# Performance work log

Measured on AMD Instinct MI355X. Metric: run time of the kernel, lower is better.

## Reference

```python
import jax, jax.numpy as jnp
import numpy as np

B, L, D, H, K = 4, 2048, 1024, 16, 3
HEAD_DIM = D // H
LN_EPS = 1e-5


def setup_inputs() -> dict:
    key = jax.random.key(0)
    ks = jax.random.split(key, 12)
    w = lambda k, shp: jax.random.normal(k, shp, jnp.float32) * (shp[-1] ** -0.5)
    return {
        "x": jax.random.normal(ks[0], (B, L, D), jnp.float32),
        "band_importance": jax.random.normal(ks[1], (1, L), jnp.float32) * 0.02,
        "Wq": w(ks[2], (D, D)), "bq": jnp.zeros((D,), jnp.float32),
        "Wk": w(ks[3], (D, D)), "bk": jnp.zeros((D,), jnp.float32),
        "Wv": w(ks[4], (D, D)), "bv": jnp.zeros((D,), jnp.float32),
        "Wo": w(ks[5], (D, D)), "bo": jnp.zeros((D,), jnp.float32),
        "gamma": jnp.ones((D,), jnp.float32),
        "beta": jnp.zeros((D,), jnp.float32),
    }


def reference(x, band_importance, Wq, bq, Wk, bk, Wv, bv, Wo, bo, gamma, beta):
    Bx, Lx, Dx = x.shape
    hd = Dx // H
    # top-k over softmax(band_importance); PyTorch bool attn_mask: True = BLOCKED
    imp = jax.nn.softmax(band_importance, axis=-1)[0]            # (L,)
    _, idx = jax.lax.top_k(imp, K)                               # (K,) int
    col_mask = jnp.zeros((Lx,), bool).at[idx].set(True)          # (L,) True -> masked out
    bias = jnp.where(col_mask, -jnp.inf, 0.0).astype(x.dtype)    # (L,)

    q = (x @ Wq.T + bq).reshape(Bx, Lx, H, hd)
    k_ = (x @ Wk.T + bk).reshape(Bx, Lx, H, hd)
    v = (x @ Wv.T + bv).reshape(Bx, Lx, H, hd)

    scale = 1.0 / np.sqrt(hd)
    scores = jnp.einsum("bqhd,bkhd->bhqk", q, k_) * scale + bias[None, None, None, :]
    attn = jax.nn.softmax(scores, axis=-1)                       # (B,H,L,L)
    ctx = jnp.einsum("bhqk,bkhd->bqhd", attn, v).reshape(Bx, Lx, Dx)
    attn_out = ctx @ Wo.T + bo

    y = x + attn_out                                             # residual
    mu = jnp.mean(y, axis=-1, keepdims=True)
    var = jnp.mean((y - mu) ** 2, axis=-1, keepdims=True)
    return (y - mu) * jax.lax.rsqrt(var + LN_EPS) * gamma + beta
```

## Files before the change

kernel.cpp:

```cpp
#include <hip/hip_runtime.h>

#define GAS __attribute__((address_space(1)))
#define LAS __attribute__((address_space(3)))

typedef __attribute__((ext_vector_type(8))) short short8;
typedef __attribute__((ext_vector_type(4))) float f32x4;
typedef __attribute__((ext_vector_type(16))) float f32x16;
typedef __attribute__((ext_vector_type(4))) unsigned int u32x4;

#define MFMA16(a,b,c) __builtin_amdgcn_mfma_f32_16x16x32_bf16(a,b,c,0,0,0)
#define MFMA32(a,b,c) __builtin_amdgcn_mfma_f32_32x32x16_bf16(a,b,c,0,0,0)

__device__ __forceinline__ unsigned short f2b(float f) {
  unsigned u = __float_as_uint(f);
  u += 0x7fffu + ((u >> 16) & 1u);
  return (unsigned short)(u >> 16);
}
__device__ __forceinline__ float b2f(unsigned short h) {
  return __uint_as_float(((unsigned)h) << 16);
}
__device__ __forceinline__ unsigned cvtpk(float a, float b) {
  unsigned r;
  asm("v_cvt_pk_bf16_f32 %0, %1, %2" : "=v"(r) : "v"(a), "v"(b));
  return r;
}
__device__ __forceinline__ void pl32swap(unsigned &x, unsigned &y) {
  auto r = __builtin_amdgcn_permlane32_swap((int)x, (int)y, false, false);
  x = (unsigned)r[0]; y = (unsigned)r[1];
}
__device__ __forceinline__ float xhalf_sum(float v) {
  auto r = __builtin_amdgcn_permlane32_swap(__float_as_int(v), __float_as_int(v), false, false);
  return __int_as_float(r[0]) + __int_as_float(r[1]);
}
__device__ __forceinline__ float fexp2(float x) {
  float r;
  asm("v_exp_f32 %0, %1" : "=v"(r) : "v"(x));
  return r;
}

union FW { u32x4 u; short8 s; };

__global__ void cvt_all(const float* __restrict__ x,
                        const float* __restrict__ Wq, const float* __restrict__ Wk,
                        const float* __restrict__ Wv, const float* __restrict__ Wo,
                        unsigned short* __restrict__ xb,
                        unsigned short* __restrict__ Wqkvb,
                        unsigned short* __restrict__ Wob) {
  const int bid = blockIdx.x;
  const float* src;
  unsigned short* dst;
  int idx;
  if (bid < 8192) {
    src = x; dst = xb; idx = bid * 256 + threadIdx.x;
  } else {
    int wb = bid - 8192;
    int seg = wb >> 10;
    idx = (wb & 1023) * 256 + threadIdx.x;
    src = (seg == 0) ? Wq : (seg == 1) ? Wk : (seg == 2) ? Wv : Wo;
    dst = (seg == 3) ? Wob : (Wqkvb + (size_t)seg * 1048576);
  }
  float4 v = reinterpret_cast<const float4*>(src)[idx];
  ushort4 o;
  o.x = f2b(v.x); o.y = f2b(v.y); o.z = f2b(v.z); o.w = f2b(v.w);
  reinterpret_cast<ushort4*>(dst)[idx] = o;
}

__global__ void topk_idx(const float* __restrict__ band, int* __restrict__ idxout) {
  __shared__ float svals[256];
  __shared__ int   sidx[256];
  __shared__ int   chosen[3];
  const int t = threadIdx.x;
  for (int pass = 0; pass < 3; ++pass) {
    float best = -INFINITY; int bi = 1 << 30;
    for (int j = t; j < 2048; j += 256) {
      float v = band[j];
      bool skip = false;
      for (int p2 = 0; p2 < pass; ++p2) skip |= (chosen[p2] == j);
      if (!skip && (v > best || (v == best && j < bi))) { best = v; bi = j; }
    }
    svals[t] = best; sidx[t] = bi;
    __syncthreads();
    for (int s = 128; s > 0; s >>= 1) {
      if (t < s) {
        float v2 = svals[t + s]; int i2 = sidx[t + s];
        if (v2 > svals[t] || (v2 == svals[t] && i2 < sidx[t])) { svals[t] = v2; sidx[t] = i2; }
      }
      __syncthreads();
    }
    if (t == 0) chosen[pass] = sidx[0];
    __syncthreads();
  }
  if (t < 3) idxout[t] = chosen[t];
}

__global__ __launch_bounds__(256) void gemm_qkv(
    const unsigned short* __restrict__ A,
    const unsigned short* __restrict__ Wqkv,
    const float* __restrict__ bq, const float* __restrict__ bk,
    const float* __restrict__ bv,
    unsigned short* __restrict__ qout, unsigned short* __restrict__ kout,
    unsigned short* __restrict__ vout, float qscale)
{
  __shared__ short As[128][64];
  __shared__ short Bs[128][64];
  const int tid = threadIdx.x;
  const int w = tid >> 6, lane = tid & 63;
  const int wm = w >> 1, wn = w & 1;
  const int flat = blockIdx.y * 64 + blockIdx.x;
  const int swb = (flat & 7) * 192 + (flat >> 3);
  const int m0 = (swb & 63) * 128, n0 = (swb >> 6) * 128;
  const int rA = lane >> 3, cA = lane & 7;

  const int seg = n0 >> 10;
  const float* biasp = (seg == 0) ? bq : (seg == 1) ? bk : bv;
  unsigned short* outp = (seg == 0) ? qout : (seg == 1) ? kout : vout;
  const float scale = (seg == 0) ? qscale : 1.0f;

  f32x4 acc[4][4];
  #pragma unroll
  for (int mt = 0; mt < 4; ++mt)
    #pragma unroll
    for (int nt = 0; nt < 4; ++nt)
      #pragma unroll
      for (int r = 0; r < 4; ++r) acc[mt][nt][r] = 0.f;

  for (int kt = 0; kt < 16; ++kt) {
    #pragma unroll
    for (int j = 0; j < 4; ++j) {
      int r = w * 32 + j * 8;
      const unsigned short* ga = A + (size_t)(m0 + r + rA) * 1024 + kt * 64 + cA * 8;
      __builtin_amdgcn_global_load_lds((const GAS void*)ga, (LAS void*)&As[r][0], 16, 0, 0);
      const unsigned short* gb = Wqkv + (size_t)(n0 + r + rA) * 1024 + kt * 64 + cA * 8;
      __builtin_amdgcn_global_load_lds((const GAS void*)gb, (LAS void*)&Bs[r][0], 16, 0, 0);
    }
    __syncthreads();
    #pragma unroll
    for (int kc = 0; kc < 2; ++kc) {
      short8 a[4], b[4];
      #pragma unroll
      for (int mt = 0; mt < 4; ++mt)
        a[mt] = *reinterpret_cast<const short8*>(
            &As[wm * 64 + mt * 16 + (lane & 15)][kc * 32 + (lane >> 4) * 8]);
      #pragma unroll
      for (int nt = 0; nt < 4; ++nt)
        b[nt] = *reinterpret_cast<const short8*>(
            &Bs[wn * 64 + nt * 16 + (lane & 15)][kc * 32 + (lane >> 4) * 8]);
      __builtin_amdgcn_s_setprio(1);
      #pragma unroll
      for (int mt = 0; mt < 4; ++mt)
        #pragma unroll
        for (int nt = 0; nt < 4; ++nt)
          acc[mt][nt] = MFMA16(a[mt], b[nt], acc[mt][nt]);
      __builtin_amdgcn_s_setprio(0);
    }
    __syncthreads();
  }
  #pragma unroll
  for (int nt = 0; nt < 4; ++nt) {
    int col = n0 + wn * 64 + nt * 16 + (lane & 15);
    int coll = col & 1023;
    float bval = biasp[coll];
    int h_ = coll >> 6, d_ = coll & 63;
    #pragma unroll
    for (int mt = 0; mt < 4; ++mt) {
      int rbase = m0 + wm * 64 + mt * 16 + ((lane >> 4) << 2);
      #pragma unroll
      for (int r = 0; r < 4; ++r) {
        unsigned short val = f2b((acc[mt][nt][r] + bval) * scale);
        int row = rbase + r;
        int b_ = row >> 11, lt_ = row & 2047;
        outp[(((size_t)(b_ * 16 + h_)) * 2048 + lt_) * 64 + d_] = val;
      }
    }
  }
}

__global__ __launch_bounds__(256) void gemm_wo(
    const unsigned short* __restrict__ A,
    const unsigned short* __restrict__ Bw,
    const float* __restrict__ bias,
    unsigned short* __restrict__ C)
{
  __shared__ short As[128][64];
  __shared__ short Bs[128][64];
  const int tid = threadIdx.x;
  const int w = tid >> 6, lane = tid & 63;
  const int wm = w >> 1, wn = w & 1;
  const int flat = blockIdx.y * 64 + blockIdx.x;
  const int swb = (flat & 7) * 64 + (flat >> 3);
  const int m0 = (swb & 63) * 128, n0 = (swb >> 6) * 128;
  const int rA = lane >> 3, cA = lane & 7;

  f32x4 acc[4][4];
  #pragma unroll
  for (int mt = 0; mt < 4; ++mt)
    #pragma unroll
    for (int nt = 0; nt < 4; ++nt)
      #pragma unroll
      for (int r = 0; r < 4; ++r) acc[mt][nt][r] = 0.f;

  for (int kt = 0; kt < 16; ++kt) {
    #pragma unroll
    for (int j = 0; j < 4; ++j) {
      int r = w * 32 + j * 8;
      const unsigned short* ga = A + (size_t)(m0 + r + rA) * 1024 + kt * 64 + cA * 8;
      __builtin_amdgcn_global_load_lds((const GAS void*)ga, (LAS void*)&As[r][0], 16, 0, 0);
      const unsigned short* gb = Bw + (size_t)(n0 + r + rA) * 1024 + kt * 64 + cA * 8;
      __builtin_amdgcn_global_load_lds((const GAS void*)gb, (LAS void*)&Bs[r][0], 16, 0, 0);
    }
    __syncthreads();
    #pragma unroll
    for (int kc = 0; kc < 2; ++kc) {
      short8 a[4], b[4];
      #pragma unroll
      for (int mt = 0; mt < 4; ++mt)
        a[mt] = *reinterpret_cast<const short8*>(
            &As[wm * 64 + mt * 16 + (lane & 15)][kc * 32 + (lane >> 4) * 8]);
      #pragma unroll
      for (int nt = 0; nt < 4; ++nt)
        b[nt] = *reinterpret_cast<const short8*>(
            &Bs[wn * 64 + nt * 16 + (lane & 15)][kc * 32 + (lane >> 4) * 8]);
      __builtin_amdgcn_s_setprio(1);
      #pragma unroll
      for (int mt = 0; mt < 4; ++mt)
        #pragma unroll
        for (int nt = 0; nt < 4; ++nt)
          acc[mt][nt] = MFMA16(a[mt], b[nt], acc[mt][nt]);
      __builtin_amdgcn_s_setprio(0);
    }
    __syncthreads();
  }
  #pragma unroll
  for (int nt = 0; nt < 4; ++nt) {
    int col = n0 + wn * 64 + nt * 16 + (lane & 15);
    float bval = bias[col];
    #pragma unroll
    for (int mt = 0; mt < 4; ++mt) {
      int rbase = m0 + wm * 64 + mt * 16 + ((lane >> 4) << 2);
      #pragma unroll
      for (int r = 0; r < 4; ++r)
        C[(size_t)(rbase + r) * 1024 + col] = f2b(acc[mt][nt][r] + bval);
    }
  }
}

__global__ __launch_bounds__(256) void transpose_v(
    const unsigned short* __restrict__ vin,
    unsigned short* __restrict__ vout)
{
  __shared__ short T[64 * 64];
  const int lt = blockIdx.x, bh = blockIdx.y;
  const int tid = threadIdx.x;
  #pragma unroll
  for (int p = 0; p < 2; ++p) {
    int id = p * 256 + tid; int l = id >> 3, c = id & 7;
    short8 v = *reinterpret_cast<const short8*>(
        vin + ((size_t)bh * 2048 + lt * 64 + l) * 64 + c * 8);
    *reinterpret_cast<short8*>(&T[l * 64 + ((c ^ (l & 7)) * 8)]) = v;
  }
  __syncthreads();
  #pragma unroll
  for (int p = 0; p < 2; ++p) {
    int id = p * 256 + tid; int d = id >> 3, c2 = id & 7;
    short8 o;
    #pragma unroll
    for (int j = 0; j < 8; ++j) {
      int l = c2 * 8 + j;
      o[j] = T[l * 64 + (((d >> 3) ^ (l & 7)) * 8) + (d & 7)];
    }
    *reinterpret_cast<short8*>(vout + ((size_t)bh * 64 + d) * 2048 + lt * 64 + c2 * 8) = o;
  }
}

#define PACK8(S, j0, OUT) {                                        \
    unsigned A_ = cvtpk(S[(j0)+0], S[(j0)+1]);                     \
    unsigned B_ = cvtpk(S[(j0)+4], S[(j0)+5]);                     \
    unsigned C_ = cvtpk(S[(j0)+2], S[(j0)+3]);                     \
    unsigned D_ = cvtpk(S[(j0)+6], S[(j0)+7]);                     \
    pl32swap(A_, B_); pl32swap(C_, D_);                            \
    FW f_; f_.u[0] = A_; f_.u[1] = C_; f_.u[2] = B_; f_.u[3] = D_; \
    OUT = f_.s; }

__global__ __launch_bounds__(256, 3) void attn4(
    const unsigned short* __restrict__ qg,
    const unsigned short* __restrict__ kg,
    const unsigned short* __restrict__ vtg,
    const int* __restrict__ midx,
    unsigned short* __restrict__ ctx)
{
  __shared__ short Ks[2][64 * 64];
  __shared__ short Vs[2][64 * 64];
  const int tid = threadIdx.x, w = tid >> 6, lane = tid & 63;
  const int flat = blockIdx.y * 16 + blockIdx.x;
  const int swzb = (flat & 7) * 128 + (flat >> 3);
  const int qt = swzb & 15, bh = swzb >> 4;
  const int q0 = qt * 128;
  const int lo5 = lane & 31, hi = lane >> 5;
  const int i0 = midx[0], i1 = midx[1], i2 = midx[2];

  const int qrow = q0 + w * 32 + lo5;
  const unsigned short* qp = qg + ((size_t)bh * 2048 + qrow) * 64 + hi * 8;
  short8 qf[4];
  #pragma unroll
  for (int ds = 0; ds < 4; ++ds) qf[ds] = *reinterpret_cast<const short8*>(qp + ds * 16);

  f32x16 oacc0, oacc1, lacc;
  #pragma unroll
  for (int r = 0; r < 16; ++r) { oacc0[r] = 0.f; oacc1[r] = 0.f; lacc[r] = 0.f; }

  const int swzoff = (((lane & 7) ^ (lane >> 3))) * 8;
  const unsigned short* kp0 =
      kg + ((size_t)bh * 2048 + w * 8 + (lane >> 3)) * 64 + swzoff;
  const unsigned short* kp1 = kp0 + 32 * 64;
  const unsigned short* vp0 =
      vtg + ((size_t)(bh * 64 + w * 8 + (lane >> 3))) * 2048 + swzoff;
  const unsigned short* vp1 = vp0 + 32 * 2048;

#define STAGE_K(bufi, tt) do {                                                 \
    __builtin_amdgcn_global_load_lds((const GAS void*)(kp0 + (tt) * 4096),     \
        (LAS void*)&Ks[bufi][(w * 8) * 64], 16, 0, 0);                         \
    __builtin_amdgcn_global_load_lds((const GAS void*)(kp1 + (tt) * 4096),     \
        (LAS void*)&Ks[bufi][(32 + w * 8) * 64], 16, 0, 0);                    \
  } while (0)
#define STAGE_V(bufi, tt) do {                                                 \
    __builtin_amdgcn_global_load_lds((const GAS void*)(vp0 + (tt) * 64),       \
        (LAS void*)&Vs[bufi][(w * 8) * 64], 16, 0, 0);                         \
    __builtin_amdgcn_global_load_lds((const GAS void*)(vp1 + (tt) * 64),       \
        (LAS void*)&Vs[bufi][(32 + w * 8) * 64], 16, 0, 0);                    \
  } while (0)

  STAGE_K(0, 0); STAGE_V(0, 0);
  STAGE_K(1, 1); STAGE_V(1, 1);

  for (int t = 0; t < 32; ++t) {
    const int buf = t & 1;
    if (t < 31) { asm volatile("s_waitcnt vmcnt(4)" ::: "memory"); }
    else        { asm volatile("s_waitcnt vmcnt(0)" ::: "memory"); }
    __builtin_amdgcn_sched_barrier(0);
    __builtin_amdgcn_s_barrier();
    __builtin_amdgcn_sched_barrier(0);

    short8 kf[8];
    #pragma unroll
    for (int ds = 0; ds < 4; ++ds) {
      int cw = ds * 2 + hi;
      kf[2 * ds] = *reinterpret_cast<const short8*>(
          &Ks[buf][lo5 * 64 + ((cw ^ (lo5 & 7)) * 8)]);
      kf[2 * ds + 1] = *reinterpret_cast<const short8*>(
          &Ks[buf][(32 + lo5) * 64 + ((cw ^ (lo5 & 7)) * 8)]);
    }
    asm volatile("s_waitcnt lgkmcnt(0)" ::: "memory");
    __builtin_amdgcn_sched_barrier(0);
    __builtin_amdgcn_s_barrier();
    __builtin_amdgcn_sched_barrier(0);
    if (t < 30) STAGE_K(buf, t + 2);

    f32x16 s0, s1;
    #pragma unroll
    for (int r = 0; r < 16; ++r) { s0[r] = 0.f; s1[r] = 0.f; }
    __builtin_amdgcn_s_setprio(1);
    #pragma unroll
    for (int ds = 0; ds < 4; ++ds) {
      s0 = MFMA32(kf[2 * ds], qf[ds], s0);
      s1 = MFMA32(kf[2 * ds + 1], qf[ds], s1);
    }
    __builtin_amdgcn_s_setprio(0);

    #pragma unroll
    for (int r = 0; r < 16; ++r) s0[r] = fexp2(s0[r]);
    #pragma unroll
    for (int r = 0; r < 16; ++r) s1[r] = fexp2(s1[r]);

    int t64 = t * 64;
    bool tm = ((unsigned)(i0 - t64) < 64u) | ((unsigned)(i1 - t64) < 64u) |
              ((unsigned)(i2 - t64) < 64u);
    if (tm) {
      #pragma unroll
      for (int r = 0; r < 16; ++r) {
        int kg0 = t64 + (r & 3) + 8 * (r >> 2) + 4 * hi;
        int kg1 = kg0 + 32;
        if (kg0 == i0 || kg0 == i1 || kg0 == i2) s0[r] = 0.f;
        if (kg1 == i0 || kg1 == i1 || kg1 == i2) s1[r] = 0.f;
      }
    }

    #pragma unroll
    for (int r = 0; r < 16; ++r) lacc[r] += s0[r] + s1[r];

    short8 pa[4];
    PACK8(s0, 0, pa[0]); PACK8(s0, 8, pa[1]);
    PACK8(s1, 0, pa[2]); PACK8(s1, 8, pa[3]);

    short8 vf[8];
    #pragma unroll
    for (int ks = 0; ks < 4; ++ks) {
      int cw = ks * 2 + hi;
      vf[2 * ks] = *reinterpret_cast<const short8*>(
          &Vs[buf][lo5 * 64 + ((cw ^ (lo5 & 7)) * 8)]);
      vf[2 * ks + 1] = *reinterpret_cast<const short8*>(
          &Vs[buf][(32 + lo5) * 64 + ((cw ^ (lo5 & 7)) * 8)]);
    }
    asm volatile("s_waitcnt lgkmcnt(0)" ::: "memory");
    __builtin_amdgcn_sched_barrier(0);
    __builtin_amdgcn_s_barrier();
    __builtin_amdgcn_sched_barrier(0);
    if (t < 30) STAGE_V(buf, t + 2);

    __builtin_amdgcn_s_setprio(1);
    #pragma unroll
    for (int ks = 0; ks < 4; ++ks) {
      oacc0 = MFMA32(pa[ks], vf[2 * ks], oacc0);
      oacc1 = MFMA32(pa[ks], vf[2 * ks + 1], oacc1);
    }
    __builtin_amdgcn_s_setprio(0);
  }

  float lsum = 0.f;
  #pragma unroll
  for (int r = 0; r < 16; ++r) lsum += lacc[r];
  lsum = xhalf_sum(lsum);
  const int bb = bh >> 4, hh = bh & 15;
  float rinv = 1.0f / lsum;
  #pragma unroll
  for (int r = 0; r < 16; ++r) {
    int row = (r & 3) + 8 * (r >> 2) + 4 * hi;
    float rv = __int_as_float(__builtin_amdgcn_ds_bpermute(
        (row + (lane & 32)) * 4, __float_as_int(rinv)));
    int qr = q0 + w * 32 + row;
    size_t base = (((size_t)(bb * 2048 + qr)) * 16 + hh) * 64;
    ctx[base + lo5]      = f2b(oacc0[r] * rv);
    ctx[base + 32 + lo5] = f2b(oacc1[r] * rv);
  }
}

__global__ __launch_bounds__(256) void resid_ln(
    const float* __restrict__ x, const unsigned short* __restrict__ ao,
    const float* __restrict__ gamma, const float* __restrict__ beta,
    float* __restrict__ out)
{
  const int row = blockIdx.x, t = threadIdx.x;
  const size_t base = (size_t)row * 1024;
  float4 xv = reinterpret_cast<const float4*>(x + base)[t];
  ushort4 av = reinterpret_cast<const ushort4*>(ao + base)[t];
  float y[4] = {xv.x + b2f(av.x), xv.y + b2f(av.y), xv.z + b2f(av.z), xv.w + b2f(av.w)};
  float sum = y[0] + y[1] + y[2] + y[3];
  float sq = y[0] * y[0] + y[1] * y[1] + y[2] * y[2] + y[3] * y[3];
  #pragma unroll
  for (int off = 1; off < 64; off <<= 1) {
    sum += __shfl_xor(sum, off);
    sq += __shfl_xor(sq, off);
  }
  __shared__ float s1[4], s2[4];
  int w = t >> 6, lane = t & 63;
  if (lane == 0) { s1[w] = sum; s2[w] = sq; }
  __syncthreads();
  sum = s1[0] + s1[1] + s1[2] + s1[3];
  sq = s2[0] + s2[1] + s2[2] + s2[3];
  float mu = sum * (1.f / 1024.f);
  float var = sq * (1.f / 1024.f) - mu * mu;
  float inv = rsqrtf(var + 1e-5f);
  float4 gv = reinterpret_cast<const float4*>(gamma)[t];
  float4 bv = reinterpret_cast<const float4*>(beta)[t];
  float4 o;
  o.x = (y[0] - mu) * inv * gv.x + bv.x;
  o.y = (y[1] - mu) * inv * gv.y + bv.y;
  o.z = (y[2] - mu) * inv * gv.z + bv.z;
  o.w = (y[3] - mu) * inv * gv.w + bv.w;
  reinterpret_cast<float4*>(out + base)[t] = o;
}

extern "C" void kernel_launch(void* const* d_in, const int* in_sizes, int n_in,
                              void* d_out, int out_size, void* d_ws, size_t ws_size,
                              hipStream_t stream)
{
  const float* x     = (const float*)d_in[0];
  const float* band  = (const float*)d_in[1];
  const float* Wq    = (const float*)d_in[2];
  const float* bq    = (const float*)d_in[3];
  const float* Wk    = (const float*)d_in[4];
  const float* bk    = (const float*)d_in[5];
  const float* Wv    = (const float*)d_in[6];
  const float* bv    = (const float*)d_in[7];
  const float* Wo    = (const float*)d_in[8];
  const float* bo    = (const float*)d_in[9];
  const float* gamma = (const float*)d_in[10];
  const float* beta  = (const float*)d_in[11];
  float* out = (float*)d_out;

  char* ws = (char*)d_ws;
  int*            idxw  = (int*)(ws);
  unsigned short* xb    = (unsigned short*)(ws + 4096);
  unsigned short* Wqkvb = (unsigned short*)(ws + 16781312);
  unsigned short* Wob   = (unsigned short*)(ws + 23072768);
  unsigned short* qb    = (unsigned short*)(ws + 25169920);
  unsigned short* kb    = (unsigned short*)(ws + 41947136);
  unsigned short* vhb   = (unsigned short*)(ws + 58724352);
  unsigned short* vtb   = (unsigned short*)(ws + 75501568);
  unsigned short* ctxb  = vhb;
  unsigned short* aob   = qb;

  const float QSCALE = 0.125f * 1.44269504f;

  cvt_all<<<12288, 256, 0, stream>>>(x, Wq, Wk, Wv, Wo, xb, Wqkvb, Wob);
  topk_idx<<<1, 256, 0, stream>>>(band, idxw);

  gemm_qkv<<<dim3(64, 24), 256, 0, stream>>>(xb, Wqkvb, bq, bk, bv,
                                             qb, kb, vhb, QSCALE);

  transpose_v<<<dim3(32, 64), 256, 0, stream>>>(vhb, vtb);

  attn4<<<dim3(16, 64), 256, 0, stream>>>(qb, kb, vtb, idxw, ctxb);

  gemm_wo<<<dim3(64, 8), 256, 0, stream>>>(ctxb, Wob, bo, aob);

  resid_ln<<<8192, 256, 0, stream>>>(x, aob, gamma, beta, out);
}
```

Baseline: 232.4 us.

## Load V fragments directly from global memory and merge top-k into convert kernel

The attention kernel stops staging V tiles through shared memory with async global-to-LDS copies. Each lane now reads its V MFMA fragments straight from global memory, issued before the QK matmul. This drops one barrier per iteration and half the LDS footprint, and the launch bound moves from 3 to 2 blocks per SM. Separately, the top-k index kernel is folded into the bf16 conversion kernel as one extra block, saving a launch. The trade-off is that V loads are no longer double-buffered and their global latency must be hidden by the QK compute, with possibly less coalesced access.

```diff
diff --git a/kernel.cpp b/kernel.cpp
--- a/kernel.cpp
+++ b/kernel.cpp
@@ -37,35 +37,40 @@
   asm("v_exp_f32 %0, %1" : "=v"(r) : "v"(x));
   return r;
 }
+__device__ __forceinline__ short8 ld8(const unsigned short* p) {
+  return *reinterpret_cast<const short8*>(p);
+}
 
 union FW { u32x4 u; short8 s; };
 
-__global__ void cvt_all(const float* __restrict__ x,
-                        const float* __restrict__ Wq, const float* __restrict__ Wk,
-                        const float* __restrict__ Wv, const float* __restrict__ Wo,
-                        unsigned short* __restrict__ xb,
-                        unsigned short* __restrict__ Wqkvb,
-                        unsigned short* __restrict__ Wob) {
+__global__ void cvt_topk(const float* __restrict__ x,
+                         const float* __restrict__ Wq, const float* __restrict__ Wk,
+                         const float* __restrict__ Wv, const float* __restrict__ Wo,
+                         const float* __restrict__ band,
+                         unsigned short* __restrict__ xb,
+                         unsigned short* __restrict__ Wqkvb,
+                         unsigned short* __restrict__ Wob,
+                         int* __restrict__ idxout) {
   const int bid = blockIdx.x;
-  const float* src;
-  unsigned short* dst;
-  int idx;
-  if (bid < 8192) {
-    src = x; dst = xb; idx = bid * 256 + threadIdx.x;
-  } else {
-    int wb = bid - 8192;
-    int seg = wb >> 10;
-    idx = (wb & 1023) * 256 + threadIdx.x;
-    src = (seg == 0) ? Wq : (seg == 1) ? Wk : (seg == 2) ? Wv : Wo;
-    dst = (seg == 3) ? Wob : (Wqkvb + (size_t)seg * 1048576);
-  }
-  float4 v = reinterpret_cast<const float4*>(src)[idx];
-  ushort4 o;
-  o.x = f2b(v.x); o.y = f2b(v.y); o.z = f2b(v.z); o.w = f2b(v.w);
-  reinterpret_cast<ushort4*>(dst)[idx] = o;
-}
-
-__global__ void topk_idx(const float* __restrict__ band, int* __restrict__ idxout) {
+  if (bid < 12288) {
+    const float* src;
+    unsigned short* dst;
+    int idx;
+    if (bid < 8192) {
+      src = x; dst = xb; idx = bid * 256 + threadIdx.x;
+    } else {
+      int wb = bid - 8192;
+      int seg = wb >> 10;
+      idx = (wb & 1023) * 256 + threadIdx.x;
+      src = (seg == 0) ? Wq : (seg == 1) ? Wk : (seg == 2) ? Wv : Wo;
+      dst = (seg == 3) ? Wob : (Wqkvb + (size_t)seg * 1048576);
+    }
+    float4 v = reinterpret_cast<const float4*>(src)[idx];
+    ushort4 o;
+    o.x = f2b(v.x); o.y = f2b(v.y); o.z = f2b(v.z); o.w = f2b(v.w);
+    reinterpret_cast<ushort4*>(dst)[idx] = o;
+    return;
+  }
   __shared__ float svals[256];
   __shared__ int   sidx[256];
   __shared__ int   chosen[3];
@@ -281,7 +286,7 @@
     FW f_; f_.u[0] = A_; f_.u[1] = C_; f_.u[2] = B_; f_.u[3] = D_; \
     OUT = f_.s; }
 
-__global__ __launch_bounds__(256, 3) void attn4(
+__global__ __launch_bounds__(256, 2) void attn5(
     const unsigned short* __restrict__ qg,
     const unsigned short* __restrict__ kg,
     const unsigned short* __restrict__ vtg,
@@ -289,7 +294,6 @@
     unsigned short* __restrict__ ctx)
 {
   __shared__ short Ks[2][64 * 64];
-  __shared__ short Vs[2][64 * 64];
   const int tid = threadIdx.x, w = tid >> 6, lane = tid & 63;
   const int flat = blockIdx.y * 16 + blockIdx.x;
   const int swzb = (flat & 7) * 128 + (flat >> 3);
@@ -312,9 +316,7 @@
   const unsigned short* kp0 =
       kg + ((size_t)bh * 2048 + w * 8 + (lane >> 3)) * 64 + swzoff;
   const unsigned short* kp1 = kp0 + 32 * 64;
-  const unsigned short* vp0 =
-      vtg + ((size_t)(bh * 64 + w * 8 + (lane >> 3))) * 2048 + swzoff;
-  const unsigned short* vp1 = vp0 + 32 * 2048;
+  const unsigned short* vbase = vtg + ((size_t)bh * 64 + lo5) * 2048 + hi * 8;
 
 #define STAGE_K(bufi, tt) do {                                                 \
     __builtin_amdgcn_global_load_lds((const GAS void*)(kp0 + (tt) * 4096),     \
@@ -322,19 +324,22 @@
     __builtin_amdgcn_global_load_lds((const GAS void*)(kp1 + (tt) * 4096),     \
         (LAS void*)&Ks[bufi][(32 + w * 8) * 64], 16, 0, 0);                    \
   } while (0)
-#define STAGE_V(bufi, tt) do {                                                 \
-    __builtin_amdgcn_global_load_lds((const GAS void*)(vp0 + (tt) * 64),       \
-        (LAS void*)&Vs[bufi][(w * 8) * 64], 16, 0, 0);                         \
-    __builtin_amdgcn_global_load_lds((const GAS void*)(vp1 + (tt) * 64),       \
-        (LAS void*)&Vs[bufi][(32 + w * 8) * 64], 16, 0, 0);                    \
+
+#define LOADV(VF, tt) do {                                                     \
+    const unsigned short* vp_ = vbase + (tt) * 64;                             \
+    VF[0] = ld8(vp_);      VF[2] = ld8(vp_ + 16);                              \
+    VF[4] = ld8(vp_ + 32); VF[6] = ld8(vp_ + 48);                              \
+    const unsigned short* vq_ = vp_ + 32 * 2048;                               \
+    VF[1] = ld8(vq_);      VF[3] = ld8(vq_ + 16);                              \
+    VF[5] = ld8(vq_ + 32); VF[7] = ld8(vq_ + 48);                              \
   } while (0)
 
-  STAGE_K(0, 0); STAGE_V(0, 0);
-  STAGE_K(1, 1); STAGE_V(1, 1);
+  STAGE_K(0, 0);
+  STAGE_K(1, 1);
 
   for (int t = 0; t < 32; ++t) {
     const int buf = t & 1;
-    if (t < 31) { asm volatile("s_waitcnt vmcnt(4)" ::: "memory"); }
+    if (t < 31) { asm volatile("s_waitcnt vmcnt(2)" ::: "memory"); }
     else        { asm volatile("s_waitcnt vmcnt(0)" ::: "memory"); }
     __builtin_amdgcn_sched_barrier(0);
     __builtin_amdgcn_s_barrier();
@@ -349,6 +354,9 @@
       kf[2 * ds + 1] = *reinterpret_cast<const short8*>(
           &Ks[buf][(32 + lo5) * 64 + ((cw ^ (lo5 & 7)) * 8)]);
     }
+    short8 vf[8];
+    LOADV(vf, t);
+
     asm volatile("s_waitcnt lgkmcnt(0)" ::: "memory");
     __builtin_amdgcn_sched_barrier(0);
     __builtin_amdgcn_s_barrier();
@@ -387,31 +395,15 @@
     #pragma unroll
     for (int r = 0; r < 16; ++r) lacc[r] += s0[r] + s1[r];
 
-    short8 pa[4];
-    PACK8(s0, 0, pa[0]); PACK8(s0, 8, pa[1]);
-    PACK8(s1, 0, pa[2]); PACK8(s1, 8, pa[3]);
-
-    short8 vf[8];
-    #pragma unroll
-    for (int ks = 0; ks < 4; ++ks) {
-      int cw = ks * 2 + hi;
-      vf[2 * ks] = *reinterpret_cast<const short8*>(
-          &Vs[buf][lo5 * 64 + ((cw ^ (lo5 & 7)) * 8)]);
-      vf[2 * ks + 1] = *reinterpret_cast<const short8*>(
-          &Vs[buf][(32 + lo5) * 64 + ((cw ^ (lo5 & 7)) * 8)]);
-    }
-    asm volatile("s_waitcnt lgkmcnt(0)" ::: "memory");
-    __builtin_amdgcn_sched_barrier(0);
-    __builtin_amdgcn_s_barrier();
-    __builtin_amdgcn_sched_barrier(0);
-    if (t < 30) STAGE_V(buf, t + 2);
+    short8 pa0, pa1, pa2, pa3;
+    PACK8(s0, 0, pa0); PACK8(s0, 8, pa1);
+    PACK8(s1, 0, pa2); PACK8(s1, 8, pa3);
 
     __builtin_amdgcn_s_setprio(1);
-    #pragma unroll
-    for (int ks = 0; ks < 4; ++ks) {
-      oacc0 = MFMA32(pa[ks], vf[2 * ks], oacc0);
-      oacc1 = MFMA32(pa[ks], vf[2 * ks + 1], oacc1);
-    }
+    oacc0 = MFMA32(pa0, vf[0], oacc0); oacc1 = MFMA32(pa0, vf[1], oacc1);
+    oacc0 = MFMA32(pa1, vf[2], oacc0); oacc1 = MFMA32(pa1, vf[3], oacc1);
+    oacc0 = MFMA32(pa2, vf[4], oacc0); oacc1 = MFMA32(pa2, vf[5], oacc1);
+    oacc0 = MFMA32(pa3, vf[6], oacc0); oacc1 = MFMA32(pa3, vf[7], oacc1);
     __builtin_amdgcn_s_setprio(0);
   }
 
@@ -501,15 +493,14 @@
 
   const float QSCALE = 0.125f * 1.44269504f;
 
-  cvt_all<<<12288, 256, 0, stream>>>(x, Wq, Wk, Wv, Wo, xb, Wqkvb, Wob);
-  topk_idx<<<1, 256, 0, stream>>>(band, idxw);
+  cvt_topk<<<12289, 256, 0, stream>>>(x, Wq, Wk, Wv, Wo, band, xb, Wqkvb, Wob, idxw);
 
   gemm_qkv<<<dim3(64, 24), 256, 0, stream>>>(xb, Wqkvb, bq, bk, bv,
                                              qb, kb, vhb, QSCALE);
 
   transpose_v<<<dim3(32, 64), 256, 0, stream>>>(vhb, vtb);
 
-  attn4<<<dim3(16, 64), 256, 0, stream>>>(qb, kb, vtb, idxw, ctxb);
+  attn5<<<dim3(16, 64), 256, 0, stream>>>(qb, kb, vtb, idxw, ctxb);
 
   gemm_wo<<<dim3(64, 8), 256, 0, stream>>>(ctxb, Wob, bo, aob);
 
```

Measured after the change: 291.2 us. 25.3% more time.

## Pipeline 256x256 QKV GEMM, emit transposed V directly, fuse topk into convert

Applied to the files above, without the earlier changes.

Replaces the 128x128 QKV GEMM with a 512-thread 256x256-tile kernel. It uses a triple-buffered LDS pipeline with swizzled global-to-LDS loads and vmcnt-based waits, so loads overlap with MFMA work. The V segment is written straight into the transposed layout, which removes the separate transpose_v kernel and its extra round trip through memory. The topk kernel is folded into the conversion kernel as one extra block, saving a launch. The bigger tiles leave fewer blocks (384) to fill the CUs and add register pressure, and the transposed V stores are narrow strided writes.

```diff
diff --git a/kernel.cpp b/kernel.cpp
--- a/kernel.cpp
+++ b/kernel.cpp
@@ -37,35 +37,40 @@
   asm("v_exp_f32 %0, %1" : "=v"(r) : "v"(x));
   return r;
 }
+__device__ __forceinline__ short8 ld8(const unsigned short* p) {
+  return *reinterpret_cast<const short8*>(p);
+}
 
 union FW { u32x4 u; short8 s; };
 
-__global__ void cvt_all(const float* __restrict__ x,
-                        const float* __restrict__ Wq, const float* __restrict__ Wk,
-                        const float* __restrict__ Wv, const float* __restrict__ Wo,
-                        unsigned short* __restrict__ xb,
-                        unsigned short* __restrict__ Wqkvb,
-                        unsigned short* __restrict__ Wob) {
+__global__ void cvt_topk(const float* __restrict__ x,
+                         const float* __restrict__ Wq, const float* __restrict__ Wk,
+                         const float* __restrict__ Wv, const float* __restrict__ Wo,
+                         const float* __restrict__ band,
+                         unsigned short* __restrict__ xb,
+                         unsigned short* __restrict__ Wqkvb,
+                         unsigned short* __restrict__ Wob,
+                         int* __restrict__ idxout) {
   const int bid = blockIdx.x;
-  const float* src;
-  unsigned short* dst;
-  int idx;
-  if (bid < 8192) {
-    src = x; dst = xb; idx = bid * 256 + threadIdx.x;
-  } else {
-    int wb = bid - 8192;
-    int seg = wb >> 10;
-    idx = (wb & 1023) * 256 + threadIdx.x;
-    src = (seg == 0) ? Wq : (seg == 1) ? Wk : (seg == 2) ? Wv : Wo;
-    dst = (seg == 3) ? Wob : (Wqkvb + (size_t)seg * 1048576);
-  }
-  float4 v = reinterpret_cast<const float4*>(src)[idx];
-  ushort4 o;
-  o.x = f2b(v.x); o.y = f2b(v.y); o.z = f2b(v.z); o.w = f2b(v.w);
-  reinterpret_cast<ushort4*>(dst)[idx] = o;
-}
-
-__global__ void topk_idx(const float* __restrict__ band, int* __restrict__ idxout) {
+  if (bid < 12288) {
+    const float* src;
+    unsigned short* dst;
+    int idx;
+    if (bid < 8192) {
+      src = x; dst = xb; idx = bid * 256 + threadIdx.x;
+    } else {
+      int wb = bid - 8192;
+      int seg = wb >> 10;
+      idx = (wb & 1023) * 256 + threadIdx.x;
+      src = (seg == 0) ? Wq : (seg == 1) ? Wk : (seg == 2) ? Wv : Wo;
+      dst = (seg == 3) ? Wob : (Wqkvb + (size_t)seg * 1048576);
+    }
+    float4 v = reinterpret_cast<const float4*>(src)[idx];
+    ushort4 o;
+    o.x = f2b(v.x); o.y = f2b(v.y); o.z = f2b(v.z); o.w = f2b(v.w);
+    reinterpret_cast<ushort4*>(dst)[idx] = o;
+    return;
+  }
   __shared__ float svals[256];
   __shared__ int   sidx[256];
   __shared__ int   chosen[3];
@@ -93,83 +98,132 @@
   if (t < 3) idxout[t] = chosen[t];
 }
 
-__global__ __launch_bounds__(256) void gemm_qkv(
+__global__ __launch_bounds__(512, 1) void gemm_qkv256(
     const unsigned short* __restrict__ A,
     const unsigned short* __restrict__ Wqkv,
     const float* __restrict__ bq, const float* __restrict__ bk,
     const float* __restrict__ bv,
     unsigned short* __restrict__ qout, unsigned short* __restrict__ kout,
-    unsigned short* __restrict__ vout, float qscale)
+    unsigned short* __restrict__ vtout, float qscale)
 {
-  __shared__ short As[128][64];
-  __shared__ short Bs[128][64];
+  __shared__ short Ls[3][2][8192];
   const int tid = threadIdx.x;
   const int w = tid >> 6, lane = tid & 63;
-  const int wm = w >> 1, wn = w & 1;
-  const int flat = blockIdx.y * 64 + blockIdx.x;
-  const int swb = (flat & 7) * 192 + (flat >> 3);
-  const int m0 = (swb & 63) * 128, n0 = (swb >> 6) * 128;
-  const int rA = lane >> 3, cA = lane & 7;
+  const int wm = w >> 2, wn = w & 3;
+  const int flat = blockIdx.y * 32 + blockIdx.x;
+  const int swb = (flat & 7) * 48 + (flat >> 3);
+  const int m0 = (swb & 31) * 256, n0 = (swb >> 5) * 256;
 
   const int seg = n0 >> 10;
   const float* biasp = (seg == 0) ? bq : (seg == 1) ? bk : bv;
-  unsigned short* outp = (seg == 0) ? qout : (seg == 1) ? kout : vout;
   const float scale = (seg == 0) ? qscale : 1.0f;
 
-  f32x4 acc[4][4];
-  #pragma unroll
-  for (int mt = 0; mt < 4; ++mt)
+  f32x4 acc[8][4];
+  #pragma unroll
+  for (int mt = 0; mt < 8; ++mt)
     #pragma unroll
     for (int nt = 0; nt < 4; ++nt)
       #pragma unroll
       for (int r = 0; r < 4; ++r) acc[mt][nt][r] = 0.f;
 
-  for (int kt = 0; kt < 16; ++kt) {
-    #pragma unroll
-    for (int j = 0; j < 4; ++j) {
-      int r = w * 32 + j * 8;
-      const unsigned short* ga = A + (size_t)(m0 + r + rA) * 1024 + kt * 64 + cA * 8;
-      __builtin_amdgcn_global_load_lds((const GAS void*)ga, (LAS void*)&As[r][0], 16, 0, 0);
-      const unsigned short* gb = Wqkv + (size_t)(n0 + r + rA) * 1024 + kt * 64 + cA * 8;
-      __builtin_amdgcn_global_load_lds((const GAS void*)gb, (LAS void*)&Bs[r][0], 16, 0, 0);
-    }
-    __syncthreads();
-    #pragma unroll
-    for (int kc = 0; kc < 2; ++kc) {
-      short8 a[4], b[4];
-      #pragma unroll
-      for (int mt = 0; mt < 4; ++mt)
-        a[mt] = *reinterpret_cast<const short8*>(
-            &As[wm * 64 + mt * 16 + (lane & 15)][kc * 32 + (lane >> 4) * 8]);
-      #pragma unroll
-      for (int nt = 0; nt < 4; ++nt)
-        b[nt] = *reinterpret_cast<const short8*>(
-            &Bs[wn * 64 + nt * 16 + (lane & 15)][kc * 32 + (lane >> 4) * 8]);
+  const int srow = tid >> 2;
+  const int scol = ((tid & 3) ^ ((srow >> 2) & 3)) * 8;
+  const unsigned short* ap = A + (size_t)(m0 + srow) * 1024 + scol;
+  const unsigned short* bp = Wqkv + (size_t)(n0 + srow) * 1024 + scol;
+  const int ldst = tid * 8;
+
+#define STG_A0(bufi, tt) __builtin_amdgcn_global_load_lds(                     \
+    (const GAS void*)(ap + (size_t)(tt) * 32), (LAS void*)&Ls[bufi][0][ldst], 16, 0, 0)
+#define STG_A1(bufi, tt) __builtin_amdgcn_global_load_lds(                     \
+    (const GAS void*)(ap + (size_t)(tt) * 32 + 131072), (LAS void*)&Ls[bufi][0][4096 + ldst], 16, 0, 0)
+#define STG_B0(bufi, tt) __builtin_amdgcn_global_load_lds(                     \
+    (const GAS void*)(bp + (size_t)(tt) * 32), (LAS void*)&Ls[bufi][1][ldst], 16, 0, 0)
+#define STG_B1(bufi, tt) __builtin_amdgcn_global_load_lds(                     \
+    (const GAS void*)(bp + (size_t)(tt) * 32 + 131072), (LAS void*)&Ls[bufi][1][4096 + ldst], 16, 0, 0)
+
+  const int r15 = lane & 15;
+  const int fcol = ((lane >> 4) * 8) ^ (((r15 >> 2) & 3) << 3);
+  const int arow0 = wm * 128 + r15;
+  const int brow0 = wn * 64 + r15;
+
+  STG_A0(0, 0); STG_A1(0, 0); STG_B0(0, 0); STG_B1(0, 0);
+  STG_A0(1, 1); STG_A1(1, 1); STG_B0(1, 1); STG_B1(1, 1);
+
+  for (int t = 0; t < 32; ++t) {
+    if (t < 31) { asm volatile("s_waitcnt vmcnt(4)" ::: "memory"); }
+    else        { asm volatile("s_waitcnt vmcnt(0)" ::: "memory"); }
+    __builtin_amdgcn_sched_barrier(0);
+    __builtin_amdgcn_s_barrier();
+    __builtin_amdgcn_sched_barrier(0);
+    const int buf = t % 3;
+    const int sbuf = (t + 2) % 3;
+    const short* Ab = &Ls[buf][0][0];
+    const short* Bb = &Ls[buf][1][0];
+
+    short8 bf[4];
+    #pragma unroll
+    for (int nt = 0; nt < 4; ++nt)
+      bf[nt] = *reinterpret_cast<const short8*>(&Bb[(brow0 + nt * 16) * 32 + fcol]);
+
+    #pragma unroll
+    for (int ph = 0; ph < 4; ++ph) {
+      if (t < 30) {
+        if (ph == 0) STG_A0(sbuf, t + 2);
+        else if (ph == 1) STG_A1(sbuf, t + 2);
+        else if (ph == 2) STG_B0(sbuf, t + 2);
+        else STG_B1(sbuf, t + 2);
+      }
+      short8 a0 = *reinterpret_cast<const short8*>(&Ab[(arow0 + (ph * 2) * 16) * 32 + fcol]);
+      short8 a1 = *reinterpret_cast<const short8*>(&Ab[(arow0 + (ph * 2 + 1) * 16) * 32 + fcol]);
       __builtin_amdgcn_s_setprio(1);
       #pragma unroll
-      for (int mt = 0; mt < 4; ++mt)
+      for (int nt = 0; nt < 4; ++nt) {
+        acc[ph * 2][nt] = MFMA16(a0, bf[nt], acc[ph * 2][nt]);
+        acc[ph * 2 + 1][nt] = MFMA16(a1, bf[nt], acc[ph * 2 + 1][nt]);
+      }
+      __builtin_amdgcn_s_setprio(0);
+    }
+
+    asm volatile("s_waitcnt lgkmcnt(0)" ::: "memory");
+    __builtin_amdgcn_sched_barrier(0);
+  }
+
+  if (seg == 2) {
+    #pragma unroll
+    for (int nt = 0; nt < 4; ++nt) {
+      int coll = (n0 + wn * 64 + nt * 16 + r15) & 1023;
+      float bval = biasp[coll];
+      int h_ = coll >> 6, d_ = coll & 63;
+      #pragma unroll
+      for (int mt = 0; mt < 8; ++mt) {
+        int rbase = m0 + wm * 128 + mt * 16 + ((lane >> 4) << 2);
+        int b_ = rbase >> 11, lt_ = rbase & 2047;
+        ushort4 pk;
+        pk.x = f2b(acc[mt][nt][0] + bval);
+        pk.y = f2b(acc[mt][nt][1] + bval);
+        pk.z = f2b(acc[mt][nt][2] + bval);
+        pk.w = f2b(acc[mt][nt][3] + bval);
+        *reinterpret_cast<ushort4*>(
+            &vtout[(((size_t)(b_ * 16 + h_)) * 64 + d_) * 2048 + lt_]) = pk;
+      }
+    }
+  } else {
+    unsigned short* outp = (seg == 0) ? qout : kout;
+    #pragma unroll
+    for (int nt = 0; nt < 4; ++nt) {
+      int coll = (n0 + wn * 64 + nt * 16 + r15) & 1023;
+      float bval = biasp[coll];
+      int h_ = coll >> 6, d_ = coll & 63;
+      #pragma unroll
+      for (int mt = 0; mt < 8; ++mt) {
+        int rbase = m0 + wm * 128 + mt * 16 + ((lane >> 4) << 2);
         #pragma unroll
-        for (int nt = 0; nt < 4; ++nt)
-          acc[mt][nt] = MFMA16(a[mt], b[nt], acc[mt][nt]);
-      __builtin_amdgcn_s_setprio(0);
-    }
-    __syncthreads();
-  }
-  #pragma unroll
-  for (int nt = 0; nt < 4; ++nt) {
-    int col = n0 + wn * 64 + nt * 16 + (lane & 15);
-    int coll = col & 1023;
-    float bval = biasp[coll];
-    int h_ = coll >> 6, d_ = coll & 63;
-    #pragma unroll
-    for (int mt = 0; mt < 4; ++mt) {
-      int rbase = m0 + wm * 64 + mt * 16 + ((lane >> 4) << 2);
-      #pragma unroll
-      for (int r = 0; r < 4; ++r) {
-        unsigned short val = f2b((acc[mt][nt][r] + bval) * scale);
-        int row = rbase + r;
-        int b_ = row >> 11, lt_ = row & 2047;
-        outp[(((size_t)(b_ * 16 + h_)) * 2048 + lt_) * 64 + d_] = val;
+        for (int r = 0; r < 4; ++r) {
+          unsigned short val = f2b((acc[mt][nt][r] + bval) * scale);
+          int row = rbase + r;
+          int b_ = row >> 11, lt_ = row & 2047;
+          outp[(((size_t)(b_ * 16 + h_)) * 2048 + lt_) * 64 + d_] = val;
+        }
       }
     }
   }
@@ -241,34 +295,6 @@
       for (int r = 0; r < 4; ++r)
         C[(size_t)(rbase + r) * 1024 + col] = f2b(acc[mt][nt][r] + bval);
     }
-  }
-}
-
-__global__ __launch_bounds__(256) void transpose_v(
-    const unsigned short* __restrict__ vin,
-    unsigned short* __restrict__ vout)
-{
-  __shared__ short T[64 * 64];
-  const int lt = blockIdx.x, bh = blockIdx.y;
-  const int tid = threadIdx.x;
-  #pragma unroll
-  for (int p = 0; p < 2; ++p) {
-    int id = p * 256 + tid; int l = id >> 3, c = id & 7;
-    short8 v = *reinterpret_cast<const short8*>(
-        vin + ((size_t)bh * 2048 + lt * 64 + l) * 64 + c * 8);
-    *reinterpret_cast<short8*>(&T[l * 64 + ((c ^ (l & 7)) * 8)]) = v;
-  }
-  __syncthreads();
-  #pragma unroll
-  for (int p = 0; p < 2; ++p) {
-    int id = p * 256 + tid; int d = id >> 3, c2 = id & 7;
-    short8 o;
-    #pragma unroll
-    for (int j = 0; j < 8; ++j) {
-      int l = c2 * 8 + j;
-      o[j] = T[l * 64 + (((d >> 3) ^ (l & 7)) * 8) + (d & 7)];
-    }
-    *reinterpret_cast<short8*>(vout + ((size_t)bh * 64 + d) * 2048 + lt * 64 + c2 * 8) = o;
   }
 }
 
@@ -302,7 +328,7 @@
   const unsigned short* qp = qg + ((size_t)bh * 2048 + qrow) * 64 + hi * 8;
   short8 qf[4];
   #pragma unroll
-  for (int ds = 0; ds < 4; ++ds) qf[ds] = *reinterpret_cast<const short8*>(qp + ds * 16);
+  for (int ds = 0; ds < 4; ++ds) qf[ds] = ld8(qp + ds * 16);
 
   f32x16 oacc0, oacc1, lacc;
   #pragma unroll
@@ -494,20 +520,16 @@
   unsigned short* Wob   = (unsigned short*)(ws + 23072768);
   unsigned short* qb    = (unsigned short*)(ws + 25169920);
   unsigned short* kb    = (unsigned short*)(ws + 41947136);
-  unsigned short* vhb   = (unsigned short*)(ws + 58724352);
+  unsigned short* ctxb  = (unsigned short*)(ws + 58724352);
   unsigned short* vtb   = (unsigned short*)(ws + 75501568);
-  unsigned short* ctxb  = vhb;
   unsigned short* aob   = qb;
 
   const float QSCALE = 0.125f * 1.44269504f;
 
-  cvt_all<<<12288, 256, 0, stream>>>(x, Wq, Wk, Wv, Wo, xb, Wqkvb, Wob);
-  topk_idx<<<1, 256, 0, stream>>>(band, idxw);
-
-  gemm_qkv<<<dim3(64, 24), 256, 0, stream>>>(xb, Wqkvb, bq, bk, bv,
-                                             qb, kb, vhb, QSCALE);
-
-  transpose_v<<<dim3(32, 64), 256, 0, stream>>>(vhb, vtb);
+  cvt_topk<<<12289, 256, 0, stream>>>(x, Wq, Wk, Wv, Wo, band, xb, Wqkvb, Wob, idxw);
+
+  gemm_qkv256<<<dim3(32, 12), 512, 0, stream>>>(xb, Wqkvb, bq, bk, bv,
+                                                qb, kb, vtb, QSCALE);
 
   attn4<<<dim3(16, 64), 256, 0, stream>>>(qb, kb, vtb, idxw, ctxb);
 
```

After: 226.4 us (median of 2 runs). 2.6% less time.
